# Kernel tuning notes

Measured on AMD Instinct MI355X. Metric: run time of the kernel, lower is better.

The kernel has to match this reference:

```python
import jax, jax.numpy as jnp
import numpy as np


def setup_inputs() -> dict:
    key = jax.random.key(0)
    ks = jax.random.split(key, 6)
    B, C, W, H = 8, 512, 64, 64
    return {
        "x": jax.random.normal(ks[0], (B, C, W, H), dtype=jnp.float32),
        "proj_query": jax.random.normal(ks[1], (C, W, H), dtype=jnp.float32),
        "key_w": jax.random.normal(ks[2], (C, C), dtype=jnp.float32) * 0.02,
        "key_b": jax.random.normal(ks[3], (C,), dtype=jnp.float32) * 0.02,
        "value_w": jax.random.normal(ks[4], (C, C), dtype=jnp.float32) * 0.02,
        "value_b": jax.random.normal(ks[5], (C,), dtype=jnp.float32) * 0.02,
        "gamma": jnp.ones((1,), dtype=jnp.float32),
    }


def reference(x, proj_query, key_w, key_b, value_w, value_b, gamma):
    B, C, W, H = x.shape
    N = W * H
    # fixed memory query: (C, N); torch builds B x N x C via permute
    q = proj_query.reshape(C, N)
    # 1x1 convs == per-pixel channel matmuls
    k = jnp.einsum('oc,bchw->bohw', key_w, x) + key_b[None, :, None, None]
    v = jnp.einsum('oc,bchw->bohw', value_w, x) + value_b[None, :, None, None]
    k = k.reshape(B, C, N)
    v = v.reshape(B, C, N)
    # energy = bmm(key [B,C,N], query^T [N,C]) -> B x C x C (channel attention)
    energy = jnp.einsum('bcn,dn->bcd', k, q)
    attention = jax.nn.softmax(energy, axis=-1)
    # out = bmm(attention^T [B,C,C], value [B,C,N]) -> B x C x N
    out = jnp.einsum('bdc,bdn->bcn', attention, v)
    out = out.reshape(B, C, W, H)
    return gamma * out + x
```

## Files before the change

kernel.cpp:

```cpp
#include <hip/hip_runtime.h>

typedef unsigned short u16;
typedef unsigned int u32;
typedef _Float16 f16x8 __attribute__((ext_vector_type(8)));
typedef float f32x4 __attribute__((ext_vector_type(4)));

#define LDST 40

__device__ __forceinline__ u16 f2h(float f) {
  union { _Float16 h; u16 u; } c; c.h = (_Float16)f; return c.u;
}
__device__ __forceinline__ float h2f(u16 v) {
  union { u16 u; _Float16 h; } c; c.u = v; return (float)c.h;
}

__device__ __forceinline__ f32x4 mfma16(f16x8 a, f16x8 b, f32x4 c) {
  return __builtin_amdgcn_mfma_f32_16x16x32_f16(a, b, c, 0, 0, 0);
}

__device__ __forceinline__ void ld8f(const float* s, u16* o) {
  float4 a = *(const float4*)s;
  float4 b = *(const float4*)(s + 4);
  o[0] = f2h(a.x); o[1] = f2h(a.y); o[2] = f2h(a.z); o[3] = f2h(a.w);
  o[4] = f2h(b.x); o[5] = f2h(b.y); o[6] = f2h(b.z); o[7] = f2h(b.w);
}

template<int TM, int TN, bool NNB>
__device__ __forceinline__ void gemm_core(const u16* A, int lda, const u16* B, int ldb,
                                          int ksteps, u16* sA, u16* sB, f32x4 acc[TM][TN]) {
  const int t = threadIdx.x;
  const int lane = t & 63, wave = t >> 6;
  const int wm = wave >> 1, wn = wave & 1;
  const int m16 = lane & 15, q4 = lane >> 4;
  constexpr int BM = TM * 32, BN = TN * 32;

  for (int kt = 0; kt < ksteps; ++kt) {
    __syncthreads();
#pragma unroll
    for (int p = 0; p < BM / 64; ++p) {
      int flat = (p * 256 + t) * 8;
      int row = flat >> 5, col = flat & 31;
      *(int4*)&sA[row * LDST + col] = *(const int4*)&A[(size_t)row * lda + col];
    }
    if constexpr (!NNB) {
#pragma unroll
      for (int p = 0; p < BN / 64; ++p) {
        int flat = (p * 256 + t) * 8;
        int row = flat >> 5, col = flat & 31;
        *(int4*)&sB[row * LDST + col] = *(const int4*)&B[(size_t)row * ldb + col];
      }
    } else {
      int kk = (t >> 4) * 2, nn = (t & 15) * 8;
      const u16* src = B + (size_t)kk * ldb + nn;
      u16 a0[8], a1[8];
      *(int4*)a0 = *(const int4*)src;
      *(int4*)a1 = *(const int4*)(src + ldb);
#pragma unroll
      for (int e = 0; e < 8; ++e) {
        int n = nn + e;
        int kf = kk ^ (((n >> 3) & 3) << 3);
        *(u32*)&sB[n * LDST + kf] = (u32)a0[e] | ((u32)a1[e] << 16);
      }
    }
    __syncthreads();

    f16x8 af[TM], bv[TN];
#pragma unroll
    for (int i = 0; i < TM; ++i)
      af[i] = *(const f16x8*)&sA[(wm * TM * 16 + i * 16 + m16) * LDST + q4 * 8];
#pragma unroll
    for (int j = 0; j < TN; ++j) {
      int n = wn * TN * 16 + j * 16 + m16;
      int kf = NNB ? ((q4 * 8) ^ (((n >> 3) & 3) << 3)) : (q4 * 8);
      bv[j] = *(const f16x8*)&sB[n * LDST + kf];
    }
#pragma unroll
    for (int i = 0; i < TM; ++i)
#pragma unroll
      for (int j = 0; j < TN; ++j)
        acc[i][j] = mfma16(af[i], bv[j], acc[i][j]);

    A += 32;
    B += NNB ? (size_t)32 * ldb : (size_t)32;
  }
}

__global__ __launch_bounds__(256) void cvt_x_kernel(const float* __restrict__ x, u16* __restrict__ xh) {
  size_t i = ((size_t)blockIdx.x * 256 + threadIdx.x) * 8;
  u16 o[8];
  ld8f(x + i, o);
  *(int4*)&xh[i] = *(int4*)o;
}

__global__ __launch_bounds__(256) void cvt_q_kernel(const float* __restrict__ q, u16* __restrict__ qh,
                                                    float* __restrict__ qs) {
  int row = blockIdx.x, t = threadIdx.x;
  float s = 0.f;
#pragma unroll
  for (int p = 0; p < 2; ++p) {
    size_t i = (size_t)row * 4096 + p * 2048 + t * 8;
    u16 o[8];
    ld8f(q + i, o);
#pragma unroll
    for (int e = 0; e < 8; ++e) s += h2f(o[e]);
    *(int4*)&qh[i] = *(int4*)o;
  }
  for (int off = 32; off; off >>= 1) s += __shfl_xor(s, off);
  __shared__ float wsum[4];
  if ((t & 63) == 0) wsum[t >> 6] = s;
  __syncthreads();
  if (t == 0) qs[row] = wsum[0] + wsum[1] + wsum[2] + wsum[3];
}

__global__ __launch_bounds__(256) void prep_kernel(const float* __restrict__ vw, u16* __restrict__ vwT,
                                                   const float* __restrict__ kw, u16* __restrict__ kwh,
                                                   float* __restrict__ beta) {
  int blk = blockIdx.x, t = threadIdx.x;
  if (blk < 256) {
    __shared__ u16 sT[32 * 33];
    int bx = blk & 15, by = blk >> 4;
#pragma unroll
    for (int p = 0; p < 4; ++p) {
      int idx = p * 256 + t; int r = idx >> 5, c = idx & 31;
      sT[r * 33 + c] = f2h(vw[(size_t)(by * 32 + r) * 512 + bx * 32 + c]);
    }
    __syncthreads();
#pragma unroll
    for (int p = 0; p < 4; ++p) {
      int idx = p * 256 + t; int r = idx >> 5, c = idx & 31;
      vwT[(size_t)(bx * 32 + r) * 512 + by * 32 + c] = sT[c * 33 + r];
    }
  } else if (blk < 384) {
    size_t i = ((size_t)(blk - 256) * 256 + t) * 8;
    u16 o[8];
    ld8f(kw + i, o);
    *(int4*)&kwh[i] = *(int4*)o;
  } else {
    for (int i = t; i < 4096; i += 256) beta[i] = 0.f;
  }
}

__global__ __launch_bounds__(256) void sgemm_kernel(const u16* __restrict__ qh, const u16* __restrict__ xh,
                                                    u16* __restrict__ Sh) {
  __shared__ u16 sA[64 * LDST], sB[64 * LDST];
  int rt = blockIdx.x, jt = blockIdx.y;
  f32x4 acc[2][2];
#pragma unroll
  for (int i = 0; i < 2; ++i)
#pragma unroll
    for (int j = 0; j < 2; ++j) acc[i][j] = (f32x4){0.f, 0.f, 0.f, 0.f};
  gemm_core<2, 2, false>(qh + (size_t)jt * 64 * 4096, 4096,
                         xh + (size_t)rt * 64 * 4096, 4096, 128, sA, sB, acc);

  const int t = threadIdx.x, lane = t & 63, wave = t >> 6;
  const int wm = wave >> 1, wn = wave & 1, m16 = lane & 15, q4 = lane >> 4;
  int b = (rt * 64) >> 9, o0 = (rt * 64) & 511;
  u16* Ob = Sh + (size_t)b * 262144;
#pragma unroll
  for (int i = 0; i < 2; ++i)
#pragma unroll
    for (int j = 0; j < 2; ++j)
#pragma unroll
      for (int r = 0; r < 4; ++r) {
        int y = jt * 64 + wm * 32 + i * 16 + q4 * 4 + r;
        int o = o0 + wn * 32 + j * 16 + m16;
        Ob[(size_t)y * 512 + o] = f2h(acc[i][j][r]);
      }
}

__global__ __launch_bounds__(256) void egemm_kernel(const u16* __restrict__ kwh, const u16* __restrict__ Sh,
                                                    float* __restrict__ E) {
  __shared__ u16 sA[64 * LDST], sB[64 * LDST];
  int xt = blockIdx.x >> 3, yt = blockIdx.x & 7, b = blockIdx.y;
  f32x4 acc[2][2];
#pragma unroll
  for (int i = 0; i < 2; ++i)
#pragma unroll
    for (int j = 0; j < 2; ++j) acc[i][j] = (f32x4){0.f, 0.f, 0.f, 0.f};
  gemm_core<2, 2, false>(kwh + (size_t)xt * 64 * 512, 512,
                         Sh + (size_t)b * 262144 + (size_t)yt * 64 * 512, 512, 16, sA, sB, acc);

  const int t = threadIdx.x, lane = t & 63, wave = t >> 6;
  const int wm = wave >> 1, wn = wave & 1, m16 = lane & 15, q4 = lane >> 4;
  float* O = E + ((size_t)b * 512 + xt * 64) * 512 + yt * 64;
#pragma unroll
  for (int i = 0; i < 2; ++i)
#pragma unroll
    for (int j = 0; j < 2; ++j)
#pragma unroll
      for (int r = 0; r < 4; ++r) {
        int row = wm * 32 + i * 16 + q4 * 4 + r;
        int col = wn * 32 + j * 16 + m16;
        O[(size_t)row * 512 + col] = acc[i][j][r];
      }
}

__global__ __launch_bounds__(256) void softmax_kernel(const float* __restrict__ E, const float* __restrict__ qs,
                                                      const float* __restrict__ kb, const float* __restrict__ vb,
                                                      u16* __restrict__ attT, float* __restrict__ beta) {
  __shared__ float sE[16 * 516];
  __shared__ float sM[16], sS[16];
  int i0 = blockIdx.x * 16, b = blockIdx.y, t = threadIdx.x;
  const float* Eb = E + ((size_t)b * 512 + i0) * 512;
  for (int ch = 0; ch < 32; ++ch) {
    int idx = ch * 256 + t;
    int row = idx >> 9, col = idx & 511;
    sE[row * 516 + col] = Eb[(size_t)row * 512 + col] + kb[i0 + row] * qs[col];
  }
  __syncthreads();
  {
    int row = t >> 4, sub = t & 15;
    float mx = -1e30f;
    for (int ii = 0; ii < 32; ++ii) mx = fmaxf(mx, sE[row * 516 + sub + ii * 16]);
    for (int off = 8; off; off >>= 1) mx = fmaxf(mx, __shfl_xor(mx, off));
    float sm = 0.f;
    for (int ii = 0; ii < 32; ++ii) sm += __expf(sE[row * 516 + sub + ii * 16] - mx);
    for (int off = 8; off; off >>= 1) sm += __shfl_xor(sm, off);
    if (sub == 0) { sM[row] = mx; sS[row] = 1.f / sm; }
  }
  __syncthreads();
  float vbr = vb[i0 + (t & 15)];
  u16* Ob = attT + (size_t)b * 262144;
  for (int ch = 0; ch < 32; ++ch) {
    int idx = ch * 256 + t;
    int r = idx & 15, j = idx >> 4;
    float a = __expf(sE[r * 516 + j] - sM[r]) * sS[r];
    Ob[(size_t)j * 512 + i0 + r] = f2h(a);
    float part = a * vbr;
    for (int off = 8; off; off >>= 1) part += __shfl_xor(part, off);
    if (r == 0) atomicAdd(&beta[b * 512 + j], part);
  }
}

__global__ __launch_bounds__(256) void wgemm_kernel(const u16* __restrict__ attT, const u16* __restrict__ vwT,
                                                    u16* __restrict__ W) {
  __shared__ u16 sA[64 * LDST], sB[64 * LDST];
  int ct = blockIdx.x >> 3, ot = blockIdx.x & 7, b = blockIdx.y;
  f32x4 acc[2][2];
#pragma unroll
  for (int i = 0; i < 2; ++i)
#pragma unroll
    for (int j = 0; j < 2; ++j) acc[i][j] = (f32x4){0.f, 0.f, 0.f, 0.f};
  gemm_core<2, 2, false>(attT + (size_t)b * 262144 + (size_t)ct * 64 * 512, 512,
                         vwT + (size_t)ot * 64 * 512, 512, 16, sA, sB, acc);

  const int t = threadIdx.x, lane = t & 63, wave = t >> 6;
  const int wm = wave >> 1, wn = wave & 1, m16 = lane & 15, q4 = lane >> 4;
  u16* O = W + (size_t)b * 262144 + (size_t)(ct * 64) * 512 + ot * 64;
#pragma unroll
  for (int i = 0; i < 2; ++i)
#pragma unroll
    for (int j = 0; j < 2; ++j)
#pragma unroll
      for (int r = 0; r < 4; ++r) {
        int row = wm * 32 + i * 16 + q4 * 4 + r;
        int col = wn * 32 + j * 16 + m16;
        O[(size_t)row * 512 + col] = f2h(acc[i][j][r]);
      }
}

__global__ __launch_bounds__(256) void outgemm_kernel(const u16* __restrict__ W, const u16* __restrict__ xh,
                                                      const float* __restrict__ x, const float* __restrict__ beta,
                                                      const float* __restrict__ gm, float* __restrict__ out) {
  __shared__ u16 sA[128 * LDST], sB[128 * LDST];
  int nt = blockIdx.x, ct = blockIdx.y, b = blockIdx.z;
  f32x4 acc[4][4];
#pragma unroll
  for (int i = 0; i < 4; ++i)
#pragma unroll
    for (int j = 0; j < 4; ++j) acc[i][j] = (f32x4){0.f, 0.f, 0.f, 0.f};
  gemm_core<4, 4, true>(W + (size_t)b * 262144 + (size_t)ct * 128 * 512, 512,
                        xh + (size_t)b * 2097152 + nt * 128, 4096, 16, sA, sB, acc);

  const int t = threadIdx.x, lane = t & 63, wave = t >> 6;
  const int wm = wave >> 1, wn = wave & 1, m16 = lane & 15, q4 = lane >> 4;
  float g = gm[0];
#pragma unroll
  for (int i = 0; i < 4; ++i)
#pragma unroll
    for (int j = 0; j < 4; ++j)
#pragma unroll
      for (int r = 0; r < 4; ++r) {
        int c = ct * 128 + wm * 64 + i * 16 + q4 * 4 + r;
        int n = nt * 128 + wn * 64 + j * 16 + m16;
        size_t idx = (size_t)b * 2097152 + (size_t)c * 4096 + n;
        out[idx] = g * (acc[i][j][r] + beta[b * 512 + c]) + x[idx];
      }
}

extern "C" void kernel_launch(void* const* d_in, const int* in_sizes, int n_in,
                              void* d_out, int out_size, void* d_ws, size_t ws_size,
                              hipStream_t stream) {
  const float* x  = (const float*)d_in[0];
  const float* pq = (const float*)d_in[1];
  const float* kw = (const float*)d_in[2];
  const float* kb = (const float*)d_in[3];
  const float* vw = (const float*)d_in[4];
  const float* vb = (const float*)d_in[5];
  const float* gm = (const float*)d_in[6];
  float* out = (float*)d_out;

  char* ws = (char*)d_ws;
  u16*   xh   = (u16*)(ws);
  u16*   qh   = (u16*)(ws + (32ull << 20));
  u16*   Sh   = (u16*)(ws + (36ull << 20));
  u16*   W    = (u16*)(ws + (36ull << 20));
  float* E    = (float*)(ws + (40ull << 20));
  u16*   attT = (u16*)(ws + (48ull << 20));
  u16*   kwh  = (u16*)(ws + (52ull << 20));
  u16*   vwT  = (u16*)(ws + (52ull << 20) + 524288);
  char*  sm   = ws + (53ull << 20);
  float* qs   = (float*)(sm);
  float* beta = (float*)(sm + 4096);

  cvt_x_kernel<<<dim3(8192), 256, 0, stream>>>(x, xh);
  cvt_q_kernel<<<dim3(512), 256, 0, stream>>>(pq, qh, qs);
  prep_kernel<<<dim3(385), 256, 0, stream>>>(vw, vwT, kw, kwh, beta);
  sgemm_kernel<<<dim3(64, 8), 256, 0, stream>>>(qh, xh, Sh);
  egemm_kernel<<<dim3(64, 8), 256, 0, stream>>>(kwh, Sh, E);
  softmax_kernel<<<dim3(32, 8), 256, 0, stream>>>(E, qs, kb, vb, attT, beta);
  wgemm_kernel<<<dim3(64, 8), 256, 0, stream>>>(attT, vwT, W);
  outgemm_kernel<<<dim3(32, 4, 8), 256, 0, stream>>>(W, xh, x, beta, gm, out);
}
```

Baseline: 262.2 us.

## Double-buffer GEMM LDS tiles with direct global-to-LDS loads and XOR swizzle

Reworks the shared GEMM core to double-buffer the A and B tiles in LDS and prefetch the next K-step while MFMAs run on the current one, leaving one barrier per step. Non-transposed operands are loaded with global_load_lds straight into an XOR-swizzled, unpadded layout. The transposed B path prefetches into registers and scatters with a rotated write order. This aims to hide global load latency and cut bank conflicts, at the cost of twice the LDS per block and more complex addressing.

```diff
diff --git a/kernel.cpp b/kernel.cpp
--- a/kernel.cpp
+++ b/kernel.cpp
@@ -2,10 +2,9 @@
 
 typedef unsigned short u16;
 typedef unsigned int u32;
+typedef unsigned long long u64;
 typedef _Float16 f16x8 __attribute__((ext_vector_type(8)));
 typedef float f32x4 __attribute__((ext_vector_type(4)));
-
-#define LDST 40
 
 __device__ __forceinline__ u16 f2h(float f) {
   union { _Float16 h; u16 u; } c; c.h = (_Float16)f; return c.u;
@@ -25,63 +24,132 @@
   o[4] = f2h(b.x); o[5] = f2h(b.y); o[6] = f2h(b.z); o[7] = f2h(b.w);
 }
 
+__device__ __forceinline__ void glds16(const u16* g, u16* l) {
+  __builtin_amdgcn_global_load_lds(
+      reinterpret_cast<const __attribute__((address_space(1))) u32*>(reinterpret_cast<u64>(g)),
+      reinterpret_cast<__attribute__((address_space(3))) u32*>(reinterpret_cast<u64>(l)),
+      16, 0, 0);
+}
+
 template<int TM, int TN, bool NNB>
-__device__ __forceinline__ void gemm_core(const u16* A, int lda, const u16* B, int ldb,
+__device__ __forceinline__ void gemm_core(const u16* __restrict__ A, int lda,
+                                          const u16* __restrict__ B, int ldb,
                                           int ksteps, u16* sA, u16* sB, f32x4 acc[TM][TN]) {
   const int t = threadIdx.x;
   const int lane = t & 63, wave = t >> 6;
   const int wm = wave >> 1, wn = wave & 1;
   const int m16 = lane & 15, q4 = lane >> 4;
   constexpr int BM = TM * 32, BN = TN * 32;
-
+  constexpr int TILEA = BM * 32, TILEB = BN * 32;
+  constexpr int APF = BM / 64;
+  constexpr int BPF = BN / 64;
+
+  int aoff[APF], asl[APF];
+#pragma unroll
+  for (int p = 0; p < APF; ++p) {
+    int s = p * 256 + t, row = s >> 2;
+    int kc = (s & 3) ^ ((row >> 1) & 3);
+    aoff[p] = row * lda + kc * 8;
+    asl[p] = (p * 256 + (t & 192)) * 8;
+  }
+  int boff[BPF], bsl[BPF];
+  if constexpr (!NNB) {
+#pragma unroll
+    for (int p = 0; p < BPF; ++p) {
+      int s = p * 256 + t, row = s >> 2;
+      int kc = (s & 3) ^ ((row >> 1) & 3);
+      boff[p] = row * ldb + kc * 8;
+      bsl[p] = (p * 256 + (t & 192)) * 8;
+    }
+  }
+
+  int aro[TM], bro[TN];
+#pragma unroll
+  for (int i = 0; i < TM; ++i) {
+    int row = wm * TM * 16 + i * 16 + m16;
+    aro[i] = row * 32 + ((q4 ^ ((row >> 1) & 3)) << 3);
+  }
+#pragma unroll
+  for (int j = 0; j < TN; ++j) {
+    int row = wn * TN * 16 + j * 16 + m16;
+    bro[j] = row * 32 + ((q4 ^ ((row >> 1) & 3)) << 3);
+  }
+
+  const int bkk = (t >> 4) * 2;
+  const int bnn = (t & 15) * 8;
+  const int erot = t & 7;
+
+#pragma unroll
+  for (int p = 0; p < APF; ++p) glds16(A + aoff[p], sA + asl[p]);
+  if constexpr (!NNB) {
+#pragma unroll
+    for (int p = 0; p < BPF; ++p) glds16(B + boff[p], sB + bsl[p]);
+  } else {
+    const u16* src = B + (size_t)bkk * ldb + bnn;
+    int4 pb0 = *(const int4*)src;
+    int4 pb1 = *(const int4*)(src + ldb);
+    u16 a0[8], a1[8];
+    *(int4*)a0 = pb0; *(int4*)a1 = pb1;
+#pragma unroll
+    for (int ee = 0; ee < 8; ++ee) {
+      int e = (ee + erot) & 7;
+      int n = bnn + e;
+      int off = n * 32 + ((((bkk >> 3) ^ ((n >> 1) & 3))) << 3) + (bkk & 7);
+      *(u32*)&sB[off] = (u32)a0[e] | ((u32)a1[e] << 16);
+    }
+  }
+  __syncthreads();
+
+  int4 nb0, nb1;
+#pragma unroll 2
   for (int kt = 0; kt < ksteps; ++kt) {
-    __syncthreads();
-#pragma unroll
-    for (int p = 0; p < BM / 64; ++p) {
-      int flat = (p * 256 + t) * 8;
-      int row = flat >> 5, col = flat & 31;
-      *(int4*)&sA[row * LDST + col] = *(const int4*)&A[(size_t)row * lda + col];
-    }
-    if constexpr (!NNB) {
-#pragma unroll
-      for (int p = 0; p < BN / 64; ++p) {
-        int flat = (p * 256 + t) * 8;
-        int row = flat >> 5, col = flat & 31;
-        *(int4*)&sB[row * LDST + col] = *(const int4*)&B[(size_t)row * ldb + col];
-      }
-    } else {
-      int kk = (t >> 4) * 2, nn = (t & 15) * 8;
-      const u16* src = B + (size_t)kk * ldb + nn;
-      u16 a0[8], a1[8];
-      *(int4*)a0 = *(const int4*)src;
-      *(int4*)a1 = *(const int4*)(src + ldb);
-#pragma unroll
-      for (int e = 0; e < 8; ++e) {
-        int n = nn + e;
-        int kf = kk ^ (((n >> 3) & 3) << 3);
-        *(u32*)&sB[n * LDST + kf] = (u32)a0[e] | ((u32)a1[e] << 16);
-      }
-    }
-    __syncthreads();
-
+    const int cur = kt & 1;
+    const int nxt = cur ^ 1;
+    const bool more = kt + 1 < ksteps;
+
+    if (more) {
+      const u16* An = A + (kt + 1) * 32;
+#pragma unroll
+      for (int p = 0; p < APF; ++p) glds16(An + aoff[p], sA + nxt * TILEA + asl[p]);
+      if constexpr (!NNB) {
+        const u16* Bn = B + (kt + 1) * 32;
+#pragma unroll
+        for (int p = 0; p < BPF; ++p) glds16(Bn + boff[p], sB + nxt * TILEB + bsl[p]);
+      } else {
+        const u16* src = B + ((size_t)(kt + 1) * 32 + bkk) * ldb + bnn;
+        nb0 = *(const int4*)src;
+        nb1 = *(const int4*)(src + ldb);
+      }
+    }
+
+    const u16* dA = sA + cur * TILEA;
+    const u16* dB = sB + cur * TILEB;
     f16x8 af[TM], bv[TN];
 #pragma unroll
-    for (int i = 0; i < TM; ++i)
-      af[i] = *(const f16x8*)&sA[(wm * TM * 16 + i * 16 + m16) * LDST + q4 * 8];
-#pragma unroll
-    for (int j = 0; j < TN; ++j) {
-      int n = wn * TN * 16 + j * 16 + m16;
-      int kf = NNB ? ((q4 * 8) ^ (((n >> 3) & 3) << 3)) : (q4 * 8);
-      bv[j] = *(const f16x8*)&sB[n * LDST + kf];
-    }
+    for (int i = 0; i < TM; ++i) af[i] = *(const f16x8*)&dA[aro[i]];
+#pragma unroll
+    for (int j = 0; j < TN; ++j) bv[j] = *(const f16x8*)&dB[bro[j]];
 #pragma unroll
     for (int i = 0; i < TM; ++i)
 #pragma unroll
       for (int j = 0; j < TN; ++j)
         acc[i][j] = mfma16(af[i], bv[j], acc[i][j]);
 
-    A += 32;
-    B += NNB ? (size_t)32 * ldb : (size_t)32;
+    if constexpr (NNB) {
+      if (more) {
+        u16 a0[8], a1[8];
+        *(int4*)a0 = nb0; *(int4*)a1 = nb1;
+        u16* wB = sB + nxt * TILEB;
+#pragma unroll
+        for (int ee = 0; ee < 8; ++ee) {
+          int e = (ee + erot) & 7;
+          int n = bnn + e;
+          int off = n * 32 + ((((bkk >> 3) ^ ((n >> 1) & 3))) << 3) + (bkk & 7);
+          *(u32*)&wB[off] = (u32)a0[e] | ((u32)a1[e] << 16);
+        }
+      }
+    }
+    __syncthreads();
   }
 }
 
@@ -142,7 +210,7 @@
 
 __global__ __launch_bounds__(256) void sgemm_kernel(const u16* __restrict__ qh, const u16* __restrict__ xh,
                                                     u16* __restrict__ Sh) {
-  __shared__ u16 sA[64 * LDST], sB[64 * LDST];
+  __shared__ __align__(16) u16 sA[2 * 64 * 32], sB[2 * 64 * 32];
   int rt = blockIdx.x, jt = blockIdx.y;
   f32x4 acc[2][2];
 #pragma unroll
@@ -170,7 +238,7 @@
 
 __global__ __launch_bounds__(256) void egemm_kernel(const u16* __restrict__ kwh, const u16* __restrict__ Sh,
                                                     float* __restrict__ E) {
-  __shared__ u16 sA[64 * LDST], sB[64 * LDST];
+  __shared__ __align__(16) u16 sA[2 * 64 * 32], sB[2 * 64 * 32];
   int xt = blockIdx.x >> 3, yt = blockIdx.x & 7, b = blockIdx.y;
   f32x4 acc[2][2];
 #pragma unroll
@@ -234,7 +302,7 @@
 
 __global__ __launch_bounds__(256) void wgemm_kernel(const u16* __restrict__ attT, const u16* __restrict__ vwT,
                                                     u16* __restrict__ W) {
-  __shared__ u16 sA[64 * LDST], sB[64 * LDST];
+  __shared__ __align__(16) u16 sA[2 * 64 * 32], sB[2 * 64 * 32];
   int ct = blockIdx.x >> 3, ot = blockIdx.x & 7, b = blockIdx.y;
   f32x4 acc[2][2];
 #pragma unroll
@@ -262,7 +330,7 @@
 __global__ __launch_bounds__(256) void outgemm_kernel(const u16* __restrict__ W, const u16* __restrict__ xh,
                                                       const float* __restrict__ x, const float* __restrict__ beta,
                                                       const float* __restrict__ gm, float* __restrict__ out) {
-  __shared__ u16 sA[128 * LDST], sB[128 * LDST];
+  __shared__ __align__(16) u16 sA[2 * 128 * 32], sB[2 * 128 * 32];
   int nt = blockIdx.x, ct = blockIdx.y, b = blockIdx.z;
   f32x4 acc[4][4];
 #pragma unroll
```

New measurement: 245.8 us. 1.07x faster.
